# Optimization experiments

Hardware: AMD Instinct MI355X
Metric: run time of the kernel (lower is better)

## Reference

```python
import jax, jax.numpy as jnp
import numpy as np
from jax import lax

B, T, D = 8, 2048, 1024


def setup_inputs() -> dict:
    key = jax.random.key(0)
    ks = jax.random.split(key, 8)
    s = 1.0 / np.sqrt(D)
    x = jax.random.normal(ks[0], (B, T, D), dtype=jnp.float32)
    Wq = jax.random.uniform(ks[1], (D, D), jnp.float32, -s, s)
    bq = jax.random.uniform(ks[2], (D,), jnp.float32, -s, s)
    Wk = jax.random.uniform(ks[3], (D, D), jnp.float32, -s, s)
    bk = jax.random.uniform(ks[4], (D,), jnp.float32, -s, s)
    Wv = jax.random.uniform(ks[5], (D, D), jnp.float32, -s, s)
    bv = jax.random.uniform(ks[6], (D,), jnp.float32, -s, s)
    decay = jnp.full((D,), 0.9, dtype=jnp.float32)  # nn.Parameter(ones*0.9)
    return {"x": x, "Wq": Wq, "bq": bq, "Wk": Wk, "bk": bk,
            "Wv": Wv, "bv": bv, "decay": decay}


def reference(x, Wq, bq, Wk, bk, Wv, bv, decay):
    # projections (torch Linear: x @ W.T + b)
    q = jnp.einsum('btd,ed->bte', x, Wq) + bq
    k = jnp.einsum('btd,ed->bte', x, Wk) + bk
    v = jnp.einsum('btd,ed->bte', x, Wv) + bv
    kv = k * v  # [B,T,D]

    # diagonal-decay linear recurrence: mem_t = decay * mem_{t-1} + kv_t
    def step(mem, kv_t):
        mem = decay * mem + kv_t  # [B,D]
        return mem, mem

    mem0 = jnp.zeros((B, D), dtype=x.dtype)
    _, mems = lax.scan(step, mem0, jnp.swapaxes(kv, 0, 1))  # mems: [T,B,D]
    out = q * jnp.swapaxes(mems, 0, 1)  # output_t = q_t * mem_t
    return out
```

## Files before the change

kernel.cpp:

```cpp
#include <hip/hip_runtime.h>
#include <cstdint>

typedef unsigned short ushort_t;
typedef __bf16 bf16x8 __attribute__((ext_vector_type(8)));
typedef float f32x4 __attribute__((ext_vector_type(4)));

#define B_ 8
#define T_ 2048
#define D_ 1024
#define M_ (B_ * T_)
#define NCHUNK 64
#define CHUNKLEN 32

__device__ __forceinline__ ushort_t f2bf(float f) {
    union { float f; uint32_t u; } v; v.f = f;
    uint32_t u = v.u;
    uint32_t r = (u + 0x7fffu + ((u >> 16) & 1u)) >> 16;
    return (ushort_t)r;
}
__device__ __forceinline__ float bf2f(ushort_t h) {
    union { uint32_t u; float f; } v; v.u = ((uint32_t)h) << 16;
    return v.f;
}
__device__ __forceinline__ uint32_t pack2bf(float lo, float hi) {
    return (uint32_t)f2bf(lo) | ((uint32_t)f2bf(hi) << 16);
}

__device__ __forceinline__ void async16(const ushort_t* g, ushort_t* l) {
    __builtin_amdgcn_global_load_lds(
        (const __attribute__((address_space(1))) void*)g,
        (__attribute__((address_space(3))) void*)l, 16, 0, 0);
}

__global__ __launch_bounds__(256) void cast_all(
    const float* __restrict__ x, const float* __restrict__ wq,
    const float* __restrict__ wk, const float* __restrict__ wv,
    ushort_t* __restrict__ xb, ushort_t* __restrict__ Wb) {
    const int nx8 = M_ * D_ / 8, nw8 = D_ * D_ / 8;
    int i = blockIdx.x * blockDim.x + threadIdx.x;
    const float* src; ushort_t* dstp; int si;
    if (i < nx8) {
        src = x; si = i; dstp = xb + (size_t)i * 8;
    } else {
        int j = i - nx8;
        dstp = Wb + (size_t)j * 8;
        if (j < nw8)          { src = wq; si = j; }
        else if (j < 2 * nw8) { src = wk; si = j - nw8; }
        else                  { src = wv; si = j - 2 * nw8; }
    }
    const float4 a = ((const float4*)src)[si * 2];
    const float4 b = ((const float4*)src)[si * 2 + 1];
    uint4 o;
    o.x = pack2bf(a.x, a.y);
    o.y = pack2bf(a.z, a.w);
    o.z = pack2bf(b.x, b.y);
    o.w = pack2bf(b.z, b.w);
    *(uint4*)dstp = o;
}

__global__ __launch_bounds__(256, 2) void gemm_qkv(
    const ushort_t* __restrict__ xb, const ushort_t* __restrict__ Wq,
    const ushort_t* __restrict__ Wk, const ushort_t* __restrict__ Wv,
    const float* __restrict__ bq, const float* __restrict__ bk,
    const float* __restrict__ bv, const float* __restrict__ decay,
    ushort_t* __restrict__ qb, ushort_t* __restrict__ kvb,
    float* __restrict__ S) {
    __shared__ ushort_t As0[128 * 32];
    __shared__ ushort_t As1[128 * 32];
    __shared__ ushort_t B00[128 * 32];
    __shared__ ushort_t B01[128 * 32];
    __shared__ ushort_t B10[128 * 32];
    __shared__ ushort_t B11[128 * 32];

    const int idx = blockIdx.x;
    const bool qmode = idx < 512;
    int mb, n0;
    const ushort_t *W0, *W1;
    if (qmode) {
        mb = idx & 127; n0 = (idx >> 7) * 256;
        W0 = Wq + (size_t)n0 * D_;
        W1 = Wq + (size_t)(n0 + 128) * D_;
    } else {
        const int j = idx - 512;
        mb = j & 127; n0 = (j >> 7) * 128;
        W0 = Wk + (size_t)n0 * D_;
        W1 = Wv + (size_t)n0 * D_;
    }
    const int m0 = mb * 128;

    const int t = threadIdx.x;
    const int lane = t & 63, wv = t >> 6;
    const int wr = (wv >> 1) * 64, wc = (wv & 1) * 64;

    f32x4 acc0[4][4], acc1[4][4];
#pragma unroll
    for (int i = 0; i < 4; ++i)
#pragma unroll
        for (int j = 0; j < 4; ++j) {
            acc0[i][j] = (f32x4){0.f, 0.f, 0.f, 0.f};
            acc1[i][j] = (f32x4){0.f, 0.f, 0.f, 0.f};
        }

    const int rs = t >> 2;
    const int g = (t & 3) ^ ((t >> 3) & 3);
    const int scol = g * 8;

    const int quad = lane >> 4;
    const int rsw = ((lane & 15) >> 1) & 3;
    const int cs = (quad ^ rsw) * 8;
    const int rowa = wr + (lane & 15);
    const int rowb = wc + (lane & 15);

#define STAGE(A_, P_, Q_, ktv)                                               \
    do {                                                                     \
        const int k0s = (ktv) * 32;                                          \
        _Pragma("unroll")                                                    \
        for (int p = 0; p < 2; ++p) {                                        \
            const int rp = rs + p * 64;                                      \
            const int Lofs = (t + p * 256) * 8;                              \
            async16(xb + (size_t)(m0 + rp) * D_ + k0s + scol, &A_[Lofs]);    \
            async16(W0 + (size_t)rp * D_ + k0s + scol, &P_[Lofs]);           \
            async16(W1 + (size_t)rp * D_ + k0s + scol, &Q_[Lofs]);           \
        }                                                                    \
    } while (0)

#define COMPUTE(A_, P_, Q_)                                                  \
    do {                                                                     \
        bf16x8 af[4], b08[4], b18[4];                                        \
        _Pragma("unroll")                                                    \
        for (int i = 0; i < 4; ++i)                                          \
            af[i] = *(const bf16x8*)&A_[(rowa + i * 16) * 32 + cs];          \
        _Pragma("unroll")                                                    \
        for (int j = 0; j < 4; ++j) {                                        \
            b08[j] = *(const bf16x8*)&P_[(rowb + j * 16) * 32 + cs];         \
            b18[j] = *(const bf16x8*)&Q_[(rowb + j * 16) * 32 + cs];         \
        }                                                                    \
        __builtin_amdgcn_s_setprio(1);                                       \
        _Pragma("unroll")                                                    \
        for (int i = 0; i < 4; ++i)                                          \
            _Pragma("unroll")                                                \
            for (int j = 0; j < 4; ++j) {                                    \
                acc0[i][j] = __builtin_amdgcn_mfma_f32_16x16x32_bf16(        \
                    af[i], b08[j], acc0[i][j], 0, 0, 0);                     \
                acc1[i][j] = __builtin_amdgcn_mfma_f32_16x16x32_bf16(        \
                    af[i], b18[j], acc1[i][j], 0, 0, 0);                     \
            }                                                                \
        __builtin_amdgcn_s_setprio(0);                                       \
    } while (0)

    STAGE(As0, B00, B10, 0);
    __syncthreads();

    for (int kt = 0; kt < 32; kt += 2) {
        STAGE(As1, B01, B11, kt + 1);
        COMPUTE(As0, B00, B10);
        __syncthreads();

        if (kt + 2 < 32) STAGE(As0, B00, B10, kt + 2);
        COMPUTE(As1, B01, B11);
        __syncthreads();
    }
#undef STAGE
#undef COMPUTE

    const int colq = lane & 15;
    const int rowq = quad * 4;

    if (qmode) {
        const float* bias0 = bq + n0;
        const float* bias1 = bq + n0 + 128;
#pragma unroll
        for (int i = 0; i < 4; ++i) {
#pragma unroll
            for (int j = 0; j < 4; ++j) {
                const int c = wc + j * 16 + colq;
                const float bv0 = bias0[c], bv1 = bias1[c];
#pragma unroll
                for (int r = 0; r < 4; ++r) {
                    const int rg = m0 + wr + i * 16 + rowq + r;
                    qb[(size_t)rg * D_ + n0 + c]       = f2bf(acc0[i][j][r] + bv0);
                    qb[(size_t)rg * D_ + n0 + 128 + c] = f2bf(acc1[i][j][r] + bv1);
                }
            }
        }
    } else {
        const float* bias0 = bk + n0;
        const float* bias1 = bv + n0;
        const int bidx = m0 >> 11;
        const int cbase = ((m0 & 2047) >> 5) + (wr >> 5);
        int cj[4];
        float bv0a[4], bv1a[4], d1a[4], d2a[4], d3a[4], P0a[4], P1a[4];
#pragma unroll
        for (int j = 0; j < 4; ++j) {
            const int c = wc + j * 16 + colq;
            cj[j] = c;
            bv0a[j] = bias0[c];
            bv1a[j] = bias1[c];
            const float dec = decay[n0 + c];
            const float d2 = dec * dec, d4 = d2 * d2;
            const float d8 = d4 * d4, d16 = d8 * d8;
            d1a[j] = dec; d2a[j] = d2; d3a[j] = d2 * dec;
            const float P1 = (quad == 0) ? (d8 * d4) : ((quad == 1) ? d8 : ((quad == 2) ? d4 : 1.0f));
            P1a[j] = P1;
            P0a[j] = d16 * P1;
        }
        float s0[4], s1[4];
#pragma unroll
        for (int j = 0; j < 4; ++j) { s0[j] = 0.f; s1[j] = 0.f; }

#pragma unroll
        for (int i = 0; i < 4; ++i) {
#pragma unroll
            for (int r = 0; r < 4; ++r) {
                const int rg = m0 + wr + i * 16 + rowq + r;
                ushort_t* rowp = kvb + (size_t)rg * D_ + n0;
#pragma unroll
                for (int j = 0; j < 4; ++j) {
                    const float kf = acc0[i][j][r] + bv0a[j];
                    const float vf = acc1[i][j][r] + bv1a[j];
                    const float kvf = kf * vf;
                    rowp[cj[j]] = f2bf(kvf);
                    const float w3 = (r == 0) ? d3a[j] : ((r == 1) ? d2a[j] : ((r == 2) ? d1a[j] : 1.0f));
                    const float wgt = ((i & 1) ? P1a[j] : P0a[j]) * w3;
                    if (i < 2) s0[j] = fmaf(kvf, wgt, s0[j]);
                    else       s1[j] = fmaf(kvf, wgt, s1[j]);
                }
            }
        }
#pragma unroll
        for (int j = 0; j < 4; ++j) {
            s0[j] += __shfl_xor(s0[j], 16, 64);
            s0[j] += __shfl_xor(s0[j], 32, 64);
            s1[j] += __shfl_xor(s1[j], 16, 64);
            s1[j] += __shfl_xor(s1[j], 32, 64);
        }
        if (quad == 0) {
#pragma unroll
            for (int j = 0; j < 4; ++j) {
                const int cg = n0 + cj[j];
                S[(((size_t)bidx * NCHUNK) + cbase) * D_ + cg]     = s0[j];
                S[(((size_t)bidx * NCHUNK) + cbase + 1) * D_ + cg] = s1[j];
            }
        }
    }
}

__global__ __launch_bounds__(128) void scan_final2(
    const ushort_t* __restrict__ kvb, const ushort_t* __restrict__ qb,
    const float* __restrict__ decay, const float* __restrict__ S,
    float* __restrict__ out) {
    const int bid = blockIdx.x;
    const int b = bid >> 7;
    const int c = (bid >> 1) & 63;
    const int dh = bid & 1;
    const int d0 = dh * 512 + threadIdx.x * 4;
    const float4 dc = *(const float4*)&decay[d0];
    float e0 = dc.x, e1 = dc.y, e2 = dc.z, e3 = dc.w;
#pragma unroll
    for (int s = 0; s < 5; ++s) { e0 *= e0; e1 *= e1; e2 *= e2; e3 *= e3; }
    float m0 = 0.f, m1 = 0.f, m2 = 0.f, m3 = 0.f;
    const float* Sb = &S[((size_t)b * NCHUNK) * D_ + d0];
    int cc = 0;
    for (; cc + 4 <= c; cc += 4) {
        const float4 sa = *(const float4*)&Sb[(size_t)(cc + 0) * D_];
        const float4 sb2 = *(const float4*)&Sb[(size_t)(cc + 1) * D_];
        const float4 sc = *(const float4*)&Sb[(size_t)(cc + 2) * D_];
        const float4 sd = *(const float4*)&Sb[(size_t)(cc + 3) * D_];
        m0 = fmaf(e0, m0, sa.x);  m1 = fmaf(e1, m1, sa.y);
        m2 = fmaf(e2, m2, sa.z);  m3 = fmaf(e3, m3, sa.w);
        m0 = fmaf(e0, m0, sb2.x); m1 = fmaf(e1, m1, sb2.y);
        m2 = fmaf(e2, m2, sb2.z); m3 = fmaf(e3, m3, sb2.w);
        m0 = fmaf(e0, m0, sc.x);  m1 = fmaf(e1, m1, sc.y);
        m2 = fmaf(e2, m2, sc.z);  m3 = fmaf(e3, m3, sc.w);
        m0 = fmaf(e0, m0, sd.x);  m1 = fmaf(e1, m1, sd.y);
        m2 = fmaf(e2, m2, sd.z);  m3 = fmaf(e3, m3, sd.w);
    }
    for (; cc < c; ++cc) {
        const float4 s4 = *(const float4*)&Sb[(size_t)cc * D_];
        m0 = fmaf(e0, m0, s4.x);
        m1 = fmaf(e1, m1, s4.y);
        m2 = fmaf(e2, m2, s4.z);
        m3 = fmaf(e3, m3, s4.w);
    }
    size_t base = ((size_t)b * T_ + c * CHUNKLEN) * D_ + d0;
#pragma unroll 8
    for (int i = 0; i < CHUNKLEN; ++i) {
        const size_t o = base + (size_t)i * D_;
        const ushort4 kv = *(const ushort4*)&kvb[o];
        const ushort4 q4 = *(const ushort4*)&qb[o];
        m0 = fmaf(dc.x, m0, bf2f(kv.x));
        m1 = fmaf(dc.y, m1, bf2f(kv.y));
        m2 = fmaf(dc.z, m2, bf2f(kv.z));
        m3 = fmaf(dc.w, m3, bf2f(kv.w));
        *(float4*)&out[o] = make_float4(bf2f(q4.x) * m0, bf2f(q4.y) * m1,
                                        bf2f(q4.z) * m2, bf2f(q4.w) * m3);
    }
}

extern "C" void kernel_launch(void* const* d_in, const int* in_sizes, int n_in,
                              void* d_out, int out_size, void* d_ws, size_t ws_size,
                              hipStream_t stream) {
    const float* x     = (const float*)d_in[0];
    const float* Wq    = (const float*)d_in[1];
    const float* bq    = (const float*)d_in[2];
    const float* Wk    = (const float*)d_in[3];
    const float* bk    = (const float*)d_in[4];
    const float* Wv    = (const float*)d_in[5];
    const float* bv    = (const float*)d_in[6];
    const float* decay = (const float*)d_in[7];
    float* out = (float*)d_out;

    char* ws = (char*)d_ws;
    ushort_t* xb  = (ushort_t*)(ws);
    ushort_t* Wb  = (ushort_t*)(ws + 33554432);
    ushort_t* qb  = (ushort_t*)(ws + 39845888);
    ushort_t* kvb = (ushort_t*)(ws + 73400320);
    float*    S   = (float*)(ws + 106954752);

    ushort_t* Wqb = Wb;
    ushort_t* Wkb = Wb + D_ * D_;
    ushort_t* Wvb = Wb + 2 * D_ * D_;

    const int ncast = (M_ * D_ / 8) + (3 * D_ * D_ / 8);
    cast_all<<<ncast / 256, 256, 0, stream>>>(x, Wq, Wk, Wv, xb, Wb);

    gemm_qkv<<<1536, 256, 0, stream>>>(xb, Wqb, Wkb, Wvb, bq, bk, bv, decay,
                                       qb, kvb, S);

    scan_final2<<<B_ * NCHUNK * 2, 128, 0, stream>>>(kvb, qb, decay, S, out);
}
```

Before: 260.9 us.

## Fuse x fp32-to-bf16 cast into QKV GEMM A-tile staging

Removes the separate cast pass over x. The GEMM now loads fp32 x rows into registers, packs them to bf16 and writes them to LDS, while the weights still use async global-to-LDS copies. This saves a 64MB read plus a 32MB write and a re-read of bf16 x. In exchange each GEMM block re-reads fp32 x, twice the bytes of bf16 x, once per N-tile block (x is re-read by several blocks), and adds register pressure plus VALU conversion work inside the main loop.

```diff
diff --git a/kernel.cpp b/kernel.cpp
--- a/kernel.cpp
+++ b/kernel.cpp
@@ -32,22 +32,16 @@
         (__attribute__((address_space(3))) void*)l, 16, 0, 0);
 }
 
-__global__ __launch_bounds__(256) void cast_all(
-    const float* __restrict__ x, const float* __restrict__ wq,
-    const float* __restrict__ wk, const float* __restrict__ wv,
-    ushort_t* __restrict__ xb, ushort_t* __restrict__ Wb) {
-    const int nx8 = M_ * D_ / 8, nw8 = D_ * D_ / 8;
-    int i = blockIdx.x * blockDim.x + threadIdx.x;
-    const float* src; ushort_t* dstp; int si;
-    if (i < nx8) {
-        src = x; si = i; dstp = xb + (size_t)i * 8;
-    } else {
-        int j = i - nx8;
-        dstp = Wb + (size_t)j * 8;
-        if (j < nw8)          { src = wq; si = j; }
-        else if (j < 2 * nw8) { src = wk; si = j - nw8; }
-        else                  { src = wv; si = j - 2 * nw8; }
-    }
+__global__ __launch_bounds__(256) void cast_w(
+    const float* __restrict__ wq, const float* __restrict__ wk,
+    const float* __restrict__ wv, ushort_t* __restrict__ Wb) {
+    const int nw8 = D_ * D_ / 8;
+    int j = blockIdx.x * blockDim.x + threadIdx.x;
+    const float* src; int si;
+    ushort_t* dstp = Wb + (size_t)j * 8;
+    if (j < nw8)          { src = wq; si = j; }
+    else if (j < 2 * nw8) { src = wk; si = j - nw8; }
+    else                  { src = wv; si = j - 2 * nw8; }
     const float4 a = ((const float4*)src)[si * 2];
     const float4 b = ((const float4*)src)[si * 2 + 1];
     uint4 o;
@@ -59,7 +53,7 @@
 }
 
 __global__ __launch_bounds__(256, 2) void gemm_qkv(
-    const ushort_t* __restrict__ xb, const ushort_t* __restrict__ Wq,
+    const float* __restrict__ xf, const ushort_t* __restrict__ Wq,
     const ushort_t* __restrict__ Wk, const ushort_t* __restrict__ Wv,
     const float* __restrict__ bq, const float* __restrict__ bk,
     const float* __restrict__ bv, const float* __restrict__ decay,
@@ -111,14 +105,38 @@
     const int rowa = wr + (lane & 15);
     const int rowb = wc + (lane & 15);
 
-#define STAGE(A_, P_, Q_, ktv)                                               \
+    const float* xr0 = xf + (size_t)(m0 + rs) * D_;
+    const float* xr1 = xf + (size_t)(m0 + rs + 64) * D_;
+
+    float4 vx0a, vx0b, vx1a, vx1b;
+
+#define STAGE_XLOAD(ktv)                                                     \
+    do {                                                                     \
+        const int kx = (ktv) * 32 + scol;                                    \
+        vx0a = *(const float4*)(xr0 + kx);                                   \
+        vx0b = *(const float4*)(xr0 + kx + 4);                               \
+        vx1a = *(const float4*)(xr1 + kx);                                   \
+        vx1b = *(const float4*)(xr1 + kx + 4);                               \
+    } while (0)
+
+#define STAGE_XWRITE(A_)                                                     \
+    do {                                                                     \
+        uint4 o0, o1;                                                        \
+        o0.x = pack2bf(vx0a.x, vx0a.y); o0.y = pack2bf(vx0a.z, vx0a.w);      \
+        o0.z = pack2bf(vx0b.x, vx0b.y); o0.w = pack2bf(vx0b.z, vx0b.w);      \
+        o1.x = pack2bf(vx1a.x, vx1a.y); o1.y = pack2bf(vx1a.z, vx1a.w);      \
+        o1.z = pack2bf(vx1b.x, vx1b.y); o1.w = pack2bf(vx1b.z, vx1b.w);      \
+        *(uint4*)&A_[t * 8] = o0;                                            \
+        *(uint4*)&A_[(t + 256) * 8] = o1;                                    \
+    } while (0)
+
+#define STAGE_W(P_, Q_, ktv)                                                 \
     do {                                                                     \
         const int k0s = (ktv) * 32;                                          \
         _Pragma("unroll")                                                    \
         for (int p = 0; p < 2; ++p) {                                        \
             const int rp = rs + p * 64;                                      \
             const int Lofs = (t + p * 256) * 8;                              \
-            async16(xb + (size_t)(m0 + rp) * D_ + k0s + scol, &A_[Lofs]);    \
             async16(W0 + (size_t)rp * D_ + k0s + scol, &P_[Lofs]);           \
             async16(W1 + (size_t)rp * D_ + k0s + scol, &Q_[Lofs]);           \
         }                                                                    \
@@ -148,19 +166,29 @@
         __builtin_amdgcn_s_setprio(0);                                       \
     } while (0)
 
-    STAGE(As0, B00, B10, 0);
+    STAGE_XLOAD(0);
+    STAGE_W(B00, B10, 0);
+    STAGE_XWRITE(As0);
     __syncthreads();
 
     for (int kt = 0; kt < 32; kt += 2) {
-        STAGE(As1, B01, B11, kt + 1);
+        STAGE_XLOAD(kt + 1);
+        STAGE_W(B01, B11, kt + 1);
         COMPUTE(As0, B00, B10);
+        STAGE_XWRITE(As1);
         __syncthreads();
 
-        if (kt + 2 < 32) STAGE(As0, B00, B10, kt + 2);
+        if (kt + 2 < 32) {
+            STAGE_XLOAD(kt + 2);
+            STAGE_W(B00, B10, kt + 2);
+        }
         COMPUTE(As1, B01, B11);
+        if (kt + 2 < 32) STAGE_XWRITE(As0);
         __syncthreads();
     }
-#undef STAGE
+#undef STAGE_XLOAD
+#undef STAGE_XWRITE
+#undef STAGE_W
 #undef COMPUTE
 
     const int colq = lane & 15;
@@ -311,20 +339,19 @@
     float* out = (float*)d_out;
 
     char* ws = (char*)d_ws;
-    ushort_t* xb  = (ushort_t*)(ws);
-    ushort_t* Wb  = (ushort_t*)(ws + 33554432);
-    ushort_t* qb  = (ushort_t*)(ws + 39845888);
-    ushort_t* kvb = (ushort_t*)(ws + 73400320);
-    float*    S   = (float*)(ws + 106954752);
+    ushort_t* Wb  = (ushort_t*)(ws);
+    ushort_t* qb  = (ushort_t*)(ws + 6291456);
+    ushort_t* kvb = (ushort_t*)(ws + 39845888);
+    float*    S   = (float*)(ws + 73400320);
 
     ushort_t* Wqb = Wb;
     ushort_t* Wkb = Wb + D_ * D_;
     ushort_t* Wvb = Wb + 2 * D_ * D_;
 
-    const int ncast = (M_ * D_ / 8) + (3 * D_ * D_ / 8);
-    cast_all<<<ncast / 256, 256, 0, stream>>>(x, Wq, Wk, Wv, xb, Wb);
-
-    gemm_qkv<<<1536, 256, 0, stream>>>(xb, Wqb, Wkb, Wvb, bq, bk, bv, decay,
+    const int ncast = 3 * D_ * D_ / 8;
+    cast_w<<<ncast / 256, 256, 0, stream>>>(Wq, Wk, Wv, Wb);
+
+    gemm_qkv<<<1536, 256, 0, stream>>>(x, Wqb, Wkb, Wvb, bq, bk, bv, decay,
                                        qb, kvb, S);
 
     scan_final2<<<B_ * NCHUNK * 2, 128, 0, stream>>>(kvb, qb, decay, S, out);
```

Result: no change. 258.5 us (-0.9%).
